# Optimization experiments

Hardware: AMD Instinct MI355X
Metric: run time of the kernel (lower is better)

The kernel has to match this reference:

```python
import jax, jax.numpy as jnp
import numpy as np

B, LQ, LA = 128, 128, 512
VOCAB, EMB, FILT, K = 50000, 300, 400, 3
EPS = 1e-8


def setup_inputs() -> dict:
    key = jax.random.key(0)
    kq, ka, ke, kw, kb, kW = jax.random.split(key, 6)
    questions = jax.random.randint(kq, (B, LQ), 0, VOCAB + 1, dtype=jnp.int32)
    answers = jax.random.randint(ka, (B, LA), 0, VOCAB + 1, dtype=jnp.int32)
    emb = jax.random.normal(ke, (VOCAB + 1, EMB), dtype=jnp.float32) * 0.1
    emb = emb.at[0].set(0.0)  # padding_idx=0
    fan_in = EMB * K
    bound = 1.0 / np.sqrt(fan_in)
    conv_w = jax.random.uniform(kw, (FILT, EMB, K), jnp.float32, -bound, bound)
    conv_b = jax.random.uniform(kb, (FILT,), jnp.float32, -bound, bound)
    W = jax.random.normal(kW, (FILT, FILT), dtype=jnp.float32)  # init.normal_(std=1)
    return {"questions": questions, "answers": answers, "emb": emb,
            "conv_w": conv_w, "conv_b": conv_b, "W": W}


def _encode(tokens, emb, conv_w, conv_b):
    # tokens [B,L] -> embed [B,L,E] -> transpose to NCH [B,E,L] -> conv1d pad=1
    x = emb[tokens].transpose(0, 2, 1)
    y = jax.lax.conv_general_dilated(
        x, conv_w, window_strides=(1,), padding=[(1, 1)],
        dimension_numbers=("NCH", "OIH", "NCH"))
    return y + conv_b[None, :, None]  # [B, FILT, L]


def reference(questions, answers, emb, conv_w, conv_b, W):
    Q = _encode(questions, emb, conv_w, conv_b)  # [B,F,Lq]
    A = _encode(answers, emb, conv_w, conv_b)    # [B,F,La]
    # G = tanh(Q^T W A)  -> [B, Lq, La]
    G = jnp.tanh(jnp.einsum("bfq,fg,bga->bqa", Q, W, A))
    roQ = jax.nn.softmax(jnp.max(G, axis=2), axis=1)  # [B,Lq]
    roA = jax.nn.softmax(jnp.max(G, axis=1), axis=1)  # [B,La]
    rQ = jnp.einsum("bfq,bq->bf", Q, roQ)  # [B,F]
    rA = jnp.einsum("bfa,ba->bf", A, roA)  # [B,F]
    nQ = jnp.maximum(jnp.linalg.norm(rQ, axis=1), EPS)
    nA = jnp.maximum(jnp.linalg.norm(rA, axis=1), EPS)
    return jnp.sum(rQ * rA, axis=1) / (nQ * nA)  # [B]
```

## Files before the change

### kernel.cpp

```cpp
#include <hip/hip_runtime.h>
#include <hip/hip_bf16.h>

#define BB   128
#define LQ   128
#define LA   512
#define EMBD 300
#define FILT 400
#define KW   3

#define NT   25
#define KC   30
#define KCF  13
#define MT   32

typedef unsigned short u16;
typedef unsigned int   u32;
typedef __attribute__((ext_vector_type(4))) int    i32x4;
typedef __attribute__((ext_vector_type(4))) float  f32x4;
typedef __attribute__((ext_vector_type(8))) __bf16 bf16x8;

__device__ __forceinline__ float b2f(u16 h){ return __uint_as_float(((u32)h) << 16); }
__device__ __forceinline__ u16 f2b(float f){
  u32 u = __float_as_uint(f);
  u32 r = (u + 0x7FFFu + ((u >> 16) & 1u)) >> 16;
  return (u16)r;
}
__device__ __forceinline__ u32 encf(float f){
  u32 u = __float_as_uint(f);
  return (u & 0x80000000u) ? ~u : (u | 0x80000000u);
}
__device__ __forceinline__ float decf(u32 k){
  u32 u = (k & 0x80000000u) ? (k ^ 0x80000000u) : ~k;
  return __uint_as_float(u);
}
__device__ __forceinline__ bf16x8 bzero(){
  i32x4 z; z.x = 0; z.y = 0; z.z = 0; z.w = 0;
  return __builtin_bit_cast(bf16x8, z);
}

__global__ void k_prep(const float* __restrict__ cw, const float* __restrict__ W,
                       u32* __restrict__ wTf, u32* __restrict__ wF){
  int idx = blockIdx.x * 256 + threadIdx.x;
  const int N1 = KC * NT * 64;
  const int N2 = KCF * NT * 64;
  if (idx < N1){
    int kc  = idx / (NT * 64);
    int rem = idx - kc * (NT * 64);
    int nt  = rem >> 6;
    int lane = rem & 63;
    int n = nt * 16 + (lane & 15);
    int quad = lane >> 4;
    u32 pack[4];
    #pragma unroll
    for (int d = 0; d < 4; d++){
      u16 h[2];
      #pragma unroll
      for (int s = 0; s < 2; s++){
        int kp = kc * 32 + quad * 8 + 2 * d + s;
        int kk = kp / 320, e = kp - kk * 320;
        float v = (e < EMBD) ? cw[(size_t)n * (EMBD * KW) + e * KW + kk] : 0.f;
        h[s] = f2b(v);
      }
      pack[d] = (u32)h[0] | ((u32)h[1] << 16);
    }
    i32x4 o; o.x = pack[0]; o.y = pack[1]; o.z = pack[2]; o.w = pack[3];
    *((i32x4*)wTf + idx) = o;
  } else if (idx < N1 + N2){
    int id2 = idx - N1;
    int kc  = id2 / (NT * 64);
    int rem = id2 - kc * (NT * 64);
    int nt  = rem >> 6;
    int lane = rem & 63;
    int n = nt * 16 + (lane & 15);
    int quad = lane >> 4;
    u32 pack[4];
    #pragma unroll
    for (int d = 0; d < 4; d++){
      u16 h[2];
      #pragma unroll
      for (int s = 0; s < 2; s++){
        int k = kc * 32 + quad * 8 + 2 * d + s;
        float v = (k < FILT) ? W[(size_t)k * FILT + n] : 0.f;
        h[s] = f2b(v);
      }
      pack[d] = (u32)h[0] | ((u32)h[1] << 16);
    }
    i32x4 o; o.x = pack[0]; o.y = pack[1]; o.z = pack[2]; o.w = pack[3];
    *((i32x4*)wF + id2) = o;
  }
}

__global__ __launch_bounds__(256) void k_encode_mfma(const int* __restrict__ toks,
    const float* __restrict__ emb, const u32* __restrict__ wTf,
    const float* __restrict__ bias, u16* __restrict__ out, int L){
  __shared__ u16 At[34 * 328];

  const int tid  = threadIdx.x;
  const int w    = tid >> 6;
  const int lane = tid & 63;
  const int col  = lane & 15;
  const int quad = lane >> 4;
  const int half = blockIdx.y;
  const int base_nt = half ? 13 : 0;
  const bool has4 = (half == 0) && (w == 0);
  const int row0 = blockIdx.x * MT;
  const int b    = row0 / L;
  const int l0   = row0 - b * L;

  int tk[10], cc[10], rws[10];
  #pragma unroll
  for (int u = 0; u < 10; u++){
    int idx = tid + 256 * u;
    tk[u] = -1; cc[u] = 0; rws[u] = 0;
    if (idx < 34 * 75){
      int r = idx / 75, c4 = idx - r * 75;
      int pos = l0 - 1 + r;
      cc[u] = c4;
      rws[u] = (r * 328 + c4 * 4) >> 1;
      if ((unsigned)pos < (unsigned)L) tk[u] = toks[b * L + pos];
    }
  }
  for (int i = tid; i < 34 * 328 / 2; i += 256) ((u32*)At)[i] = 0u;
  __syncthreads();
  {
    const float4* emb4 = (const float4*)emb;
    float4 v[10];
    #pragma unroll
    for (int u = 0; u < 10; u++)
      if (tk[u] >= 0) v[u] = emb4[(size_t)tk[u] * 75 + cc[u]];
    #pragma unroll
    for (int u = 0; u < 10; u++){
      if (tk[u] >= 0){
        u32 p0 = (u32)f2b(v[u].x) | ((u32)f2b(v[u].y) << 16);
        u32 p1 = (u32)f2b(v[u].z) | ((u32)f2b(v[u].w) << 16);
        ((u32*)At)[rws[u]]     = p0;
        ((u32*)At)[rws[u] + 1] = p1;
      }
    }
  }

  f32x4 acc[4][2];
  #pragma unroll
  for (int j = 0; j < 4; j++)
    #pragma unroll
    for (int mf = 0; mf < 2; mf++)
      acc[j][mf] = (f32x4){0.f, 0.f, 0.f, 0.f};

  __syncthreads();

  const i32x4* bbase = (const i32x4*)wTf + (size_t)(base_nt + w) * 64 + lane;
  i32x4 Bb[2][4];
  i32x4 Ab[2][2];
  {
    #pragma unroll
    for (int j = 0; j < 3; j++) Bb[0][j] = bbase[(4 * j) * 64];
    if (has4) Bb[0][3] = bbase[12 * 64];
    const int ebase0 = quad * 8;
    Ab[0][0] = *(const i32x4*)(At + (col) * 328 + ebase0);
    Ab[0][1] = *(const i32x4*)(At + (16 + col) * 328 + ebase0);
  }
  #pragma unroll
  for (int kc = 0; kc < KC; kc++){
    const int cur = kc & 1;
    if (kc + 1 < KC){
      const i32x4* s = bbase + (size_t)(kc + 1) * (NT * 64);
      #pragma unroll
      for (int j = 0; j < 3; j++) Bb[cur ^ 1][j] = s[(4 * j) * 64];
      if (has4) Bb[cur ^ 1][3] = s[12 * 64];
      const int kk1 = (kc + 1) / 10, e01 = ((kc + 1) - kk1 * 10) * 32;
      const int ebase1 = e01 + quad * 8;
      Ab[cur ^ 1][0] = *(const i32x4*)(At + (col + kk1) * 328 + ebase1);
      Ab[cur ^ 1][1] = *(const i32x4*)(At + (16 + col + kk1) * 328 + ebase1);
    }
    bf16x8 a0 = __builtin_bit_cast(bf16x8, Ab[cur][0]);
    bf16x8 a1 = __builtin_bit_cast(bf16x8, Ab[cur][1]);
    #pragma unroll
    for (int j = 0; j < 3; j++){
      bf16x8 bf = __builtin_bit_cast(bf16x8, Bb[cur][j]);
      acc[j][0] = __builtin_amdgcn_mfma_f32_16x16x32_bf16(a0, bf, acc[j][0], 0, 0, 0);
      acc[j][1] = __builtin_amdgcn_mfma_f32_16x16x32_bf16(a1, bf, acc[j][1], 0, 0, 0);
    }
    if (has4){
      bf16x8 bf = __builtin_bit_cast(bf16x8, Bb[cur][3]);
      acc[3][0] = __builtin_amdgcn_mfma_f32_16x16x32_bf16(a0, bf, acc[3][0], 0, 0, 0);
      acc[3][1] = __builtin_amdgcn_mfma_f32_16x16x32_bf16(a1, bf, acc[3][1], 0, 0, 0);
    }
  }

  #pragma unroll
  for (int j = 0; j < 4; j++){
    if (j == 3 && !has4) continue;
    int n = (base_nt + w + 4 * j) * 16 + col;
    float bv = bias[n];
    #pragma unroll
    for (int mf = 0; mf < 2; mf++){
      int rbase = row0 + mf * 16 + quad * 4;
      #pragma unroll
      for (int r = 0; r < 4; r++)
        out[(size_t)(rbase + r) * FILT + n] = f2b(acc[j][mf][r] + bv);
    }
  }
}

__global__ __launch_bounds__(256) void k_gemmT3(const u16* __restrict__ QT,
    const u32* __restrict__ wF, u16* __restrict__ T){
  const int tid  = threadIdx.x;
  const int w    = tid >> 6;
  const int lane = tid & 63;
  const int col  = lane & 15;
  const int quad = lane >> 4;
  const int half = blockIdx.y;
  const int base_nt = half ? 13 : 0;
  const bool has4 = (half == 0) && (w == 0);
  const int row0 = blockIdx.x * MT;

  f32x4 acc[4][2];
  #pragma unroll
  for (int j = 0; j < 4; j++)
    #pragma unroll
    for (int mf = 0; mf < 2; mf++)
      acc[j][mf] = (f32x4){0.f, 0.f, 0.f, 0.f};

  const u16* arow0 = QT + (size_t)(row0 + col) * FILT;
  const u16* arow1 = QT + (size_t)(row0 + 16 + col) * FILT;
  const i32x4* bbase = (const i32x4*)wF + (size_t)(base_nt + w) * 64 + lane;

  i32x4 Ab[2][2];
  i32x4 Bb[2][4];
  {
    int off = quad * 8;
    Ab[0][0] = *(const i32x4*)(arow0 + off);
    Ab[0][1] = *(const i32x4*)(arow1 + off);
    #pragma unroll
    for (int j = 0; j < 3; j++) Bb[0][j] = bbase[(4 * j) * 64];
    if (has4) Bb[0][3] = bbase[12 * 64];
  }
  #pragma unroll
  for (int kc = 0; kc < KCF; kc++){
    const int cur = kc & 1;
    if (kc + 1 < KCF){
      int off = (kc + 1) * 32 + quad * 8;
      Ab[cur ^ 1][0] = *(const i32x4*)(arow0 + off);
      Ab[cur ^ 1][1] = *(const i32x4*)(arow1 + off);
      const i32x4* s = bbase + (size_t)(kc + 1) * (NT * 64);
      #pragma unroll
      for (int j = 0; j < 3; j++) Bb[cur ^ 1][j] = s[(4 * j) * 64];
      if (has4) Bb[cur ^ 1][3] = s[12 * 64];
    }
    bf16x8 a0 = __builtin_bit_cast(bf16x8, Ab[cur][0]);
    bf16x8 a1 = __builtin_bit_cast(bf16x8, Ab[cur][1]);
    #pragma unroll
    for (int j = 0; j < 3; j++){
      bf16x8 bf = __builtin_bit_cast(bf16x8, Bb[cur][j]);
      acc[j][0] = __builtin_amdgcn_mfma_f32_16x16x32_bf16(a0, bf, acc[j][0], 0, 0, 0);
      acc[j][1] = __builtin_amdgcn_mfma_f32_16x16x32_bf16(a1, bf, acc[j][1], 0, 0, 0);
    }
    if (has4){
      bf16x8 bf = __builtin_bit_cast(bf16x8, Bb[cur][3]);
      acc[3][0] = __builtin_amdgcn_mfma_f32_16x16x32_bf16(a0, bf, acc[3][0], 0, 0, 0);
      acc[3][1] = __builtin_amdgcn_mfma_f32_16x16x32_bf16(a1, bf, acc[3][1], 0, 0, 0);
    }
  }

  #pragma unroll
  for (int j = 0; j < 4; j++){
    if (j == 3 && !has4) continue;
    int n = (base_nt + w + 4 * j) * 16 + col;
    #pragma unroll
    for (int mf = 0; mf < 2; mf++){
      int rbase = row0 + mf * 16 + quad * 4;
      #pragma unroll
      for (int r = 0; r < 4; r++)
        T[(size_t)(rbase + r) * FILT + n] = f2b(acc[j][mf][r]);
    }
  }
}

__global__ __launch_bounds__(256) void k_scores3(const u16* __restrict__ T,
    const u16* __restrict__ AT, u32* __restrict__ rowmaxE, u32* __restrict__ colmaxE){
  __shared__ float rpart[64][17];
  __shared__ float cpart[128][17];
  const int tid  = threadIdx.x;
  const int w    = tid >> 6;
  const int lane = tid & 63;
  const int col  = lane & 15;
  const int quad = lane >> 4;
  const int b    = blockIdx.y;
  const int a0   = blockIdx.x * 128;
  const int qt   = blockIdx.z * 4 + w;

  f32x4 acc[8];
  #pragma unroll
  for (int j = 0; j < 8; j++) acc[j] = (f32x4){0.f, 0.f, 0.f, 0.f};

  const u16* tr = T  + (size_t)(b * LQ + qt * 16 + col) * FILT;
  const u16* ar = AT + (size_t)(b * LA + a0 + col) * FILT;

  i32x4 Abuf[2], Bbuf[2][8];
  {
    int off = quad * 8;
    Abuf[0] = *(const i32x4*)(tr + off);
    #pragma unroll
    for (int j = 0; j < 8; j++)
      Bbuf[0][j] = *(const i32x4*)(ar + (size_t)(j * 16) * FILT + off);
  }
  #pragma unroll
  for (int kc = 0; kc < KCF; kc++){
    const int cur = kc & 1;
    if (kc + 1 < KCF){
      int off = (kc + 1) * 32 + quad * 8;
      Abuf[cur ^ 1] = *(const i32x4*)(tr + off);
      #pragma unroll
      for (int j = 0; j < 8; j++)
        Bbuf[cur ^ 1][j] = *(const i32x4*)(ar + (size_t)(j * 16) * FILT + off);
    }
    const bool live = (kc < 12) || (quad < 2);
    bf16x8 a0 = live ? __builtin_bit_cast(bf16x8, Abuf[cur]) : bzero();
    #pragma unroll
    for (int j = 0; j < 8; j++){
      bf16x8 bf = __builtin_bit_cast(bf16x8, Bbuf[cur][j]);
      acc[j] = __builtin_amdgcn_mfma_f32_16x16x32_bf16(a0, bf, acc[j], 0, 0, 0);
    }
  }

  #pragma unroll
  for (int r = 0; r < 4; r++){
    float m = acc[0][r];
    #pragma unroll
    for (int j = 1; j < 8; j++) m = fmaxf(m, acc[j][r]);
    rpart[w * 16 + quad * 4 + r][col] = m;
  }
  #pragma unroll
  for (int j = 0; j < 8; j++){
    float m = acc[j][0];
    #pragma unroll
    for (int r = 1; r < 4; r++) m = fmaxf(m, acc[j][r]);
    cpart[j * 16 + col][w * 4 + quad] = m;
  }
  __syncthreads();
  if (tid < 64){
    float m = rpart[tid][0];
    #pragma unroll
    for (int g = 1; g < 16; g++) m = fmaxf(m, rpart[tid][g]);
    atomicMax(&rowmaxE[b * LQ + blockIdx.z * 64 + tid], encf(m));
  } else if (tid < 192){
    int a = tid - 64;
    float m2 = cpart[a][0];
    #pragma unroll
    for (int g = 1; g < 16; g++) m2 = fmaxf(m2, cpart[a][g]);
    atomicMax(&colmaxE[b * LA + a0 + a], encf(m2));
  }
  if (tid >= 192 && tid < 256){
    int a = tid - 128;
    float m2 = cpart[a][0];
    #pragma unroll
    for (int g = 1; g < 16; g++) m2 = fmaxf(m2, cpart[a][g]);
    atomicMax(&colmaxE[b * LA + a0 + a], encf(m2));
  }
}

__global__ __launch_bounds__(256) void k_soft(const u32* __restrict__ rme,
    const u32* __restrict__ cme, float* __restrict__ roq, float* __restrict__ roa){
  __shared__ float sq[128];
  __shared__ float sa[512];
  __shared__ float red[4];
  int b = blockIdx.x, tid = threadIdx.x;
  if (tid < 128) sq[tid] = tanhf(decf(rme[b * LQ + tid]));
  sa[tid]       = tanhf(decf(cme[b * LA + tid]));
  sa[tid + 256] = tanhf(decf(cme[b * LA + 256 + tid]));
  __syncthreads();
  if (tid < 64){
    float m = fmaxf(sq[tid], sq[tid + 64]);
    #pragma unroll
    for (int off = 32; off; off >>= 1) m = fmaxf(m, __shfl_down(m, off));
    if (tid == 0) red[0] = m;
  } else if (tid < 128){
    int l = tid - 64;
    float m = sa[l];
    #pragma unroll
    for (int i = 1; i < 8; i++) m = fmaxf(m, sa[l + 64 * i]);
    #pragma unroll
    for (int off = 32; off; off >>= 1) m = fmaxf(m, __shfl_down(m, off));
    if (l == 0) red[1] = m;
  }
  __syncthreads();
  float mq = red[0], ma = red[1];
  if (tid < 128) sq[tid] = __expf(sq[tid] - mq);
  sa[tid]       = __expf(sa[tid] - ma);
  sa[tid + 256] = __expf(sa[tid + 256] - ma);
  __syncthreads();
  if (tid < 64){
    float s = sq[tid] + sq[tid + 64];
    #pragma unroll
    for (int off = 32; off; off >>= 1) s += __shfl_down(s, off);
    if (tid == 0) red[2] = s;
  } else if (tid < 128){
    int l = tid - 64;
    float s = 0.f;
    #pragma unroll
    for (int i = 0; i < 8; i++) s += sa[l + 64 * i];
    #pragma unroll
    for (int off = 32; off; off >>= 1) s += __shfl_down(s, off);
    if (l == 0) red[3] = s;
  }
  __syncthreads();
  float iq = 1.f / red[2], ia = 1.f / red[3];
  if (tid < 128) roq[b * LQ + tid] = sq[tid] * iq;
  roa[b * LA + tid]       = sa[tid] * ia;
  roa[b * LA + 256 + tid] = sa[tid + 256] * ia;
}

__global__ __launch_bounds__(256) void k_pool(const u16* __restrict__ QT,
    const u16* __restrict__ AT, const float* __restrict__ roq, const float* __restrict__ roa,
    float* __restrict__ rqp, float* __restrict__ rap){
  __shared__ float wq[32];
  __shared__ float wa[128];
  int s = blockIdx.x, b = blockIdx.y, tid = threadIdx.x;
  if (tid < 32) wq[tid] = roq[b * LQ + s * 32 + tid];
  if (tid >= 128 && tid < 256) wa[tid - 128] = roa[b * LA + s * 128 + (tid - 128)];
  __syncthreads();
  if (tid < FILT / 2){
    const u32* qp = (const u32*)(QT + (size_t)(b * LQ + s * 32) * FILT) + tid;
    const u32* ap = (const u32*)(AT + (size_t)(b * LA + s * 128) * FILT) + tid;
    float rq0 = 0.f, rq1 = 0.f, ra0 = 0.f, ra1 = 0.f;
    for (int q = 0; q < 32; q++){
      u32 u = qp[q * (FILT / 2)];
      float wv = wq[q];
      rq0 += __uint_as_float(u << 16) * wv;
      rq1 += __uint_as_float(u & 0xFFFF0000u) * wv;
    }
    for (int a = 0; a < 128; a++){
      u32 u = ap[a * (FILT / 2)];
      float wv = wa[a];
      ra0 += __uint_as_float(u << 16) * wv;
      ra1 += __uint_as_float(u & 0xFFFF0000u) * wv;
    }
    size_t base = ((size_t)b * 4 + s) * FILT + 2 * tid;
    rqp[base] = rq0; rqp[base + 1] = rq1;
    rap[base] = ra0; rap[base + 1] = ra1;
  }
}

__global__ __launch_bounds__(256) void k_cos(const float* __restrict__ rqp,
    const float* __restrict__ rap, float* __restrict__ outp){
  __shared__ float rd[4], r1[4], r2[4];
  int b = blockIdx.x, tid = threadIdx.x;
  int lane = tid & 63, w = tid >> 6;
  float d = 0.f, n1 = 0.f, n2 = 0.f;
  for (int f = tid; f < FILT; f += 256){
    size_t base = (size_t)b * 4 * FILT + f;
    float rq = rqp[base] + rqp[base + FILT] + rqp[base + 2 * FILT] + rqp[base + 3 * FILT];
    float ra = rap[base] + rap[base + FILT] + rap[base + 2 * FILT] + rap[base + 3 * FILT];
    d += rq * ra; n1 += rq * rq; n2 += ra * ra;
  }
  #pragma unroll
  for (int off = 32; off; off >>= 1){
    d  += __shfl_down(d, off);
    n1 += __shfl_down(n1, off);
    n2 += __shfl_down(n2, off);
  }
  if (lane == 0){ rd[w] = d; r1[w] = n1; r2[w] = n2; }
  __syncthreads();
  if (tid == 0){
    float D  = rd[0] + rd[1] + rd[2] + rd[3];
    float N1 = r1[0] + r1[1] + r1[2] + r1[3];
    float N2 = r2[0] + r2[1] + r2[2] + r2[3];
    outp[b] = D / (fmaxf(sqrtf(N1), 1e-8f) * fmaxf(sqrtf(N2), 1e-8f));
  }
}

extern "C" void kernel_launch(void* const* d_in, const int* in_sizes, int n_in,
                              void* d_out, int out_size, void* d_ws, size_t ws_size,
                              hipStream_t stream){
  const int*   qtok = (const int*)d_in[0];
  const int*   atok = (const int*)d_in[1];
  const float* emb  = (const float*)d_in[2];
  const float* cw   = (const float*)d_in[3];
  const float* cb   = (const float*)d_in[4];
  const float* W    = (const float*)d_in[5];
  float* outp = (float*)d_out;

  char* ws = (char*)d_ws;
  size_t off = 0;
  auto alloc = [&](size_t bytes) -> char* {
    char* p = ws + off;
    off = (off + bytes + 255) & ~(size_t)255;
    return p;
  };
  u32*   wTf = (u32*)alloc((size_t)KC * NT * 64 * 16);
  u32*   wF  = (u32*)alloc((size_t)KCF * NT * 64 * 16);
  u16*   QT  = (u16*)alloc((size_t)BB * LQ * FILT * 2);
  u16*   AT  = (u16*)alloc((size_t)BB * LA * FILT * 2);
  u16*   T   = (u16*)alloc((size_t)BB * LQ * FILT * 2);
  u32*   rme = (u32*)alloc((size_t)BB * LQ * 4);
  u32*   cme = (u32*)alloc((size_t)BB * LA * 4);
  float* roq = (float*)alloc((size_t)BB * LQ * 4);
  float* roa = (float*)alloc((size_t)BB * LA * 4);
  float* rqp = (float*)alloc((size_t)BB * 4 * FILT * 4);
  float* rap = (float*)alloc((size_t)BB * 4 * FILT * 4);

  hipMemsetAsync(rme, 0, (size_t)BB * LQ * 4 + (size_t)BB * LA * 4, stream);

  const int NPREP = KC * NT * 64 + KCF * NT * 64;
  k_prep<<<dim3((NPREP + 255) / 256), 256, 0, stream>>>(cw, W, wTf, wF);
  k_encode_mfma<<<dim3(BB * LQ / MT, 2), 256, 0, stream>>>(qtok, emb, wTf, cb, QT, LQ);
  k_encode_mfma<<<dim3(BB * LA / MT, 2), 256, 0, stream>>>(atok, emb, wTf, cb, AT, LA);
  k_gemmT3<<<dim3(BB * LQ / MT, 2), 256, 0, stream>>>(QT, wF, T);
  k_scores3<<<dim3(LA / 128, BB, 2), 256, 0, stream>>>(T, AT, rme, cme);
  k_soft<<<dim3(BB), 256, 0, stream>>>(rme, cme, roq, roa);
  k_pool<<<dim3(4, BB), 256, 0, stream>>>(QT, AT, roq, roa, rqp, rap);
  k_cos<<<dim3(BB), 256, 0, stream>>>(rqp, rap, outp);
}
```

Measured before the change: 265.4 us.

## Fuse W-projection into score kernel and merge softmax, pooling, cosine tail

Replaces the separate Q·W GEMM and score kernels with one kernel. It computes the projected Q tile into shared memory and immediately multiplies it against A rows to produce row and column maxima. This removes the global T buffer round trip. The softmax, weighted pooling and cosine kernels are merged into a single per-batch kernel, removing intermediate global buffers and launches. The cost is that each (z, qh) block recomputes its Q·W tile twice across z, and the grid is now 512 blocks, which may limit parallelism.

```diff
diff --git a/kernel.cpp b/kernel.cpp
--- a/kernel.cpp
+++ b/kernel.cpp
@@ -19,7 +19,6 @@
 typedef __attribute__((ext_vector_type(4))) float  f32x4;
 typedef __attribute__((ext_vector_type(8))) __bf16 bf16x8;
 
-__device__ __forceinline__ float b2f(u16 h){ return __uint_as_float(((u32)h) << 16); }
 __device__ __forceinline__ u16 f2b(float f){
   u32 u = __float_as_uint(f);
   u32 r = (u + 0x7FFFu + ((u >> 16) & 1u)) >> 16;
@@ -202,256 +201,206 @@
   }
 }
 
-__global__ __launch_bounds__(256) void k_gemmT3(const u16* __restrict__ QT,
-    const u32* __restrict__ wF, u16* __restrict__ T){
+__global__ __launch_bounds__(512) void k_mid(const u16* __restrict__ QT,
+    const u32* __restrict__ wF, const u16* __restrict__ AT,
+    u32* __restrict__ rme, u32* __restrict__ cme){
+  __shared__ u16 Ts[64 * 408];
+  __shared__ float cpart[256][5];
   const int tid  = threadIdx.x;
   const int w    = tid >> 6;
   const int lane = tid & 63;
   const int col  = lane & 15;
   const int quad = lane >> 4;
-  const int half = blockIdx.y;
-  const int base_nt = half ? 13 : 0;
-  const bool has4 = (half == 0) && (w == 0);
-  const int row0 = blockIdx.x * MT;
-
-  f32x4 acc[4][2];
-  #pragma unroll
-  for (int j = 0; j < 4; j++)
-    #pragma unroll
-    for (int mf = 0; mf < 2; mf++)
-      acc[j][mf] = (f32x4){0.f, 0.f, 0.f, 0.f};
-
-  const u16* arow0 = QT + (size_t)(row0 + col) * FILT;
-  const u16* arow1 = QT + (size_t)(row0 + 16 + col) * FILT;
-  const i32x4* bbase = (const i32x4*)wF + (size_t)(base_nt + w) * 64 + lane;
-
-  i32x4 Ab[2][2];
-  i32x4 Bb[2][4];
+  const int z    = blockIdx.x;
+  const int qh   = blockIdx.y;
+  const int b    = blockIdx.z;
+  const int wq   = w & 3;
+  const int wh   = w >> 2;
+
   {
-    int off = quad * 8;
-    Ab[0][0] = *(const i32x4*)(arow0 + off);
-    Ab[0][1] = *(const i32x4*)(arow1 + off);
-    #pragma unroll
-    for (int j = 0; j < 3; j++) Bb[0][j] = bbase[(4 * j) * 64];
-    if (has4) Bb[0][3] = bbase[12 * 64];
-  }
-  #pragma unroll
-  for (int kc = 0; kc < KCF; kc++){
-    const int cur = kc & 1;
-    if (kc + 1 < KCF){
-      int off = (kc + 1) * 32 + quad * 8;
-      Ab[cur ^ 1][0] = *(const i32x4*)(arow0 + off);
-      Ab[cur ^ 1][1] = *(const i32x4*)(arow1 + off);
-      const i32x4* s = bbase + (size_t)(kc + 1) * (NT * 64);
-      #pragma unroll
-      for (int j = 0; j < 3; j++) Bb[cur ^ 1][j] = s[(4 * j) * 64];
-      if (has4) Bb[cur ^ 1][3] = s[12 * 64];
-    }
-    bf16x8 a0 = __builtin_bit_cast(bf16x8, Ab[cur][0]);
-    bf16x8 a1 = __builtin_bit_cast(bf16x8, Ab[cur][1]);
-    #pragma unroll
-    for (int j = 0; j < 3; j++){
-      bf16x8 bf = __builtin_bit_cast(bf16x8, Bb[cur][j]);
-      acc[j][0] = __builtin_amdgcn_mfma_f32_16x16x32_bf16(a0, bf, acc[j][0], 0, 0, 0);
-      acc[j][1] = __builtin_amdgcn_mfma_f32_16x16x32_bf16(a1, bf, acc[j][1], 0, 0, 0);
-    }
-    if (has4){
-      bf16x8 bf = __builtin_bit_cast(bf16x8, Bb[cur][3]);
-      acc[3][0] = __builtin_amdgcn_mfma_f32_16x16x32_bf16(a0, bf, acc[3][0], 0, 0, 0);
-      acc[3][1] = __builtin_amdgcn_mfma_f32_16x16x32_bf16(a1, bf, acc[3][1], 0, 0, 0);
-    }
-  }
-
-  #pragma unroll
-  for (int j = 0; j < 4; j++){
-    if (j == 3 && !has4) continue;
-    int n = (base_nt + w + 4 * j) * 16 + col;
-    #pragma unroll
-    for (int mf = 0; mf < 2; mf++){
-      int rbase = row0 + mf * 16 + quad * 4;
-      #pragma unroll
-      for (int r = 0; r < 4; r++)
-        T[(size_t)(rbase + r) * FILT + n] = f2b(acc[j][mf][r]);
-    }
-  }
-}
-
-__global__ __launch_bounds__(256) void k_scores3(const u16* __restrict__ T,
-    const u16* __restrict__ AT, u32* __restrict__ rowmaxE, u32* __restrict__ colmaxE){
-  __shared__ float rpart[64][17];
-  __shared__ float cpart[128][17];
-  const int tid  = threadIdx.x;
-  const int w    = tid >> 6;
-  const int lane = tid & 63;
-  const int col  = lane & 15;
-  const int quad = lane >> 4;
-  const int b    = blockIdx.y;
-  const int a0   = blockIdx.x * 128;
-  const int qt   = blockIdx.z * 4 + w;
-
-  f32x4 acc[8];
-  #pragma unroll
-  for (int j = 0; j < 8; j++) acc[j] = (f32x4){0.f, 0.f, 0.f, 0.f};
-
-  const u16* tr = T  + (size_t)(b * LQ + qt * 16 + col) * FILT;
-  const u16* ar = AT + (size_t)(b * LA + a0 + col) * FILT;
-
-  i32x4 Abuf[2], Bbuf[2][8];
+    const int bnt = wh ? 13 : 0;
+    const int cnt = wh ? 12 : 13;
+    const u16* arow = QT + (size_t)(b * LQ + qh * 64 + wq * 16 + col) * FILT;
+    const i32x4* wFp = (const i32x4*)wF;
+    for (int ntc = 0; ntc < 3; ntc++){
+      const int nleft = cnt - ntc * 5;
+      f32x4 acc[5];
+      #pragma unroll
+      for (int j = 0; j < 5; j++) acc[j] = (f32x4){0.f, 0.f, 0.f, 0.f};
+      i32x4 Ab[2], Bb[2][5];
+      Ab[0] = *(const i32x4*)(arow + quad * 8);
+      #pragma unroll
+      for (int j = 0; j < 5; j++)
+        if (j < nleft) Bb[0][j] = wFp[(size_t)(bnt + ntc * 5 + j) * 64 + lane];
+      for (int kc = 0; kc < KCF; kc++){
+        const int cur = kc & 1;
+        if (kc + 1 < KCF){
+          Ab[cur ^ 1] = *(const i32x4*)(arow + (kc + 1) * 32 + quad * 8);
+          #pragma unroll
+          for (int j = 0; j < 5; j++)
+            if (j < nleft)
+              Bb[cur ^ 1][j] = wFp[((size_t)(kc + 1) * NT + bnt + ntc * 5 + j) * 64 + lane];
+        }
+        bf16x8 a = __builtin_bit_cast(bf16x8, Ab[cur]);
+        #pragma unroll
+        for (int j = 0; j < 5; j++)
+          if (j < nleft)
+            acc[j] = __builtin_amdgcn_mfma_f32_16x16x32_bf16(a,
+                       __builtin_bit_cast(bf16x8, Bb[cur][j]), acc[j], 0, 0, 0);
+      }
+      #pragma unroll
+      for (int j = 0; j < 5; j++){
+        if (j < nleft){
+          int g = (bnt + ntc * 5 + j) * 16 + col;
+          #pragma unroll
+          for (int r = 0; r < 4; r++)
+            Ts[(wq * 16 + quad * 4 + r) * 408 + g] = f2b(acc[j][r]);
+        }
+      }
+    }
+  }
+  __syncthreads();
+
+  float rm[4];
+  #pragma unroll
+  for (int r = 0; r < 4; r++) rm[r] = -3.4e38f;
+  const u16* Tsrow = Ts + (wq * 16 + col) * 408;
+  for (int atg = 0; atg < 2; atg++){
+    f32x4 acc[4];
+    #pragma unroll
+    for (int i = 0; i < 4; i++) acc[i] = (f32x4){0.f, 0.f, 0.f, 0.f};
+    const u16* ar[4];
+    #pragma unroll
+    for (int i = 0; i < 4; i++)
+      ar[i] = AT + (size_t)(b * LA + z * 256 + (wh * 8 + atg * 4 + i) * 16 + col) * FILT;
+    i32x4 Ab2[2], Bb2[2][4];
+    Ab2[0] = *(const i32x4*)(Tsrow + quad * 8);
+    #pragma unroll
+    for (int i = 0; i < 4; i++) Bb2[0][i] = *(const i32x4*)(ar[i] + quad * 8);
+    for (int kc = 0; kc < KCF; kc++){
+      const int cur = kc & 1;
+      if (kc + 1 < KCF){
+        int off = (kc + 1) * 32 + quad * 8;
+        Ab2[cur ^ 1] = *(const i32x4*)(Tsrow + off);
+        #pragma unroll
+        for (int i = 0; i < 4; i++) Bb2[cur ^ 1][i] = *(const i32x4*)(ar[i] + off);
+      }
+      const bool live = (kc < 12) || (quad < 2);
+      bf16x8 a = live ? __builtin_bit_cast(bf16x8, Ab2[cur]) : bzero();
+      #pragma unroll
+      for (int i = 0; i < 4; i++)
+        acc[i] = __builtin_amdgcn_mfma_f32_16x16x32_bf16(a,
+                   __builtin_bit_cast(bf16x8, Bb2[cur][i]), acc[i], 0, 0, 0);
+    }
+    #pragma unroll
+    for (int i = 0; i < 4; i++){
+      float cmx = fmaxf(fmaxf(acc[i][0], acc[i][1]), fmaxf(acc[i][2], acc[i][3]));
+      cmx = fmaxf(cmx, __shfl_xor(cmx, 16));
+      cmx = fmaxf(cmx, __shfl_xor(cmx, 32));
+      if (quad == 0) cpart[(wh * 8 + atg * 4 + i) * 16 + col][wq] = cmx;
+      #pragma unroll
+      for (int r = 0; r < 4; r++) rm[r] = fmaxf(rm[r], acc[i][r]);
+    }
+  }
+  #pragma unroll
+  for (int r = 0; r < 4; r++){
+    float m = rm[r];
+    m = fmaxf(m, __shfl_xor(m, 1));
+    m = fmaxf(m, __shfl_xor(m, 2));
+    m = fmaxf(m, __shfl_xor(m, 4));
+    m = fmaxf(m, __shfl_xor(m, 8));
+    if (col == 0)
+      atomicMax(&rme[b * LQ + qh * 64 + wq * 16 + quad * 4 + r], encf(m));
+  }
+  __syncthreads();
+  if (tid < 256){
+    float m = cpart[tid][0];
+    #pragma unroll
+    for (int s = 1; s < 4; s++) m = fmaxf(m, cpart[tid][s]);
+    atomicMax(&cme[b * LA + z * 256 + tid], encf(m));
+  }
+}
+
+__global__ __launch_bounds__(512) void k_tail(const u16* __restrict__ QT,
+    const u16* __restrict__ AT, const u32* __restrict__ rme,
+    const u32* __restrict__ cme, float* __restrict__ outp){
+  __shared__ float roq[128];
+  __shared__ float roa[512];
+  __shared__ float red[4];
+  __shared__ float rqp[8][400];
+  __shared__ float rap[8][400];
+  __shared__ float fin[8][3];
+  const int tid = threadIdx.x, w = tid >> 6, lane = tid & 63;
+  const int b = blockIdx.x;
+  if (tid < 128) roq[tid] = tanhf(decf(rme[b * LQ + tid]));
+  roa[tid] = tanhf(decf(cme[b * LA + tid]));
+  __syncthreads();
+  if (w == 0){
+    float m = fmaxf(roq[lane], roq[lane + 64]);
+    #pragma unroll
+    for (int off = 32; off; off >>= 1) m = fmaxf(m, __shfl_down(m, off));
+    if (lane == 0) red[0] = m;
+  } else if (w == 1){
+    float m = roa[lane];
+    #pragma unroll
+    for (int i = 1; i < 8; i++) m = fmaxf(m, roa[lane + 64 * i]);
+    #pragma unroll
+    for (int off = 32; off; off >>= 1) m = fmaxf(m, __shfl_down(m, off));
+    if (lane == 0) red[1] = m;
+  }
+  __syncthreads();
+  if (tid < 128) roq[tid] = __expf(roq[tid] - red[0]);
+  roa[tid] = __expf(roa[tid] - red[1]);
+  __syncthreads();
+  if (w == 0){
+    float s = roq[lane] + roq[lane + 64];
+    #pragma unroll
+    for (int off = 32; off; off >>= 1) s += __shfl_down(s, off);
+    if (lane == 0) red[2] = s;
+  } else if (w == 1){
+    float s = 0.f;
+    #pragma unroll
+    for (int i = 0; i < 8; i++) s += roa[lane + 64 * i];
+    #pragma unroll
+    for (int off = 32; off; off >>= 1) s += __shfl_down(s, off);
+    if (lane == 0) red[3] = s;
+  }
+  __syncthreads();
+  if (tid < 128) roq[tid] *= (1.f / red[2]);
+  roa[tid] *= (1.f / red[3]);
+  __syncthreads();
   {
-    int off = quad * 8;
-    Abuf[0] = *(const i32x4*)(tr + off);
-    #pragma unroll
-    for (int j = 0; j < 8; j++)
-      Bbuf[0][j] = *(const i32x4*)(ar + (size_t)(j * 16) * FILT + off);
-  }
-  #pragma unroll
-  for (int kc = 0; kc < KCF; kc++){
-    const int cur = kc & 1;
-    if (kc + 1 < KCF){
-      int off = (kc + 1) * 32 + quad * 8;
-      Abuf[cur ^ 1] = *(const i32x4*)(tr + off);
-      #pragma unroll
-      for (int j = 0; j < 8; j++)
-        Bbuf[cur ^ 1][j] = *(const i32x4*)(ar + (size_t)(j * 16) * FILT + off);
-    }
-    const bool live = (kc < 12) || (quad < 2);
-    bf16x8 a0 = live ? __builtin_bit_cast(bf16x8, Abuf[cur]) : bzero();
-    #pragma unroll
-    for (int j = 0; j < 8; j++){
-      bf16x8 bf = __builtin_bit_cast(bf16x8, Bbuf[cur][j]);
-      acc[j] = __builtin_amdgcn_mfma_f32_16x16x32_bf16(a0, bf, acc[j], 0, 0, 0);
-    }
-  }
-
-  #pragma unroll
-  for (int r = 0; r < 4; r++){
-    float m = acc[0][r];
-    #pragma unroll
-    for (int j = 1; j < 8; j++) m = fmaxf(m, acc[j][r]);
-    rpart[w * 16 + quad * 4 + r][col] = m;
-  }
-  #pragma unroll
-  for (int j = 0; j < 8; j++){
-    float m = acc[j][0];
-    #pragma unroll
-    for (int r = 1; r < 4; r++) m = fmaxf(m, acc[j][r]);
-    cpart[j * 16 + col][w * 4 + quad] = m;
-  }
-  __syncthreads();
-  if (tid < 64){
-    float m = rpart[tid][0];
-    #pragma unroll
-    for (int g = 1; g < 16; g++) m = fmaxf(m, rpart[tid][g]);
-    atomicMax(&rowmaxE[b * LQ + blockIdx.z * 64 + tid], encf(m));
-  } else if (tid < 192){
-    int a = tid - 64;
-    float m2 = cpart[a][0];
-    #pragma unroll
-    for (int g = 1; g < 16; g++) m2 = fmaxf(m2, cpart[a][g]);
-    atomicMax(&colmaxE[b * LA + a0 + a], encf(m2));
-  }
-  if (tid >= 192 && tid < 256){
-    int a = tid - 128;
-    float m2 = cpart[a][0];
-    #pragma unroll
-    for (int g = 1; g < 16; g++) m2 = fmaxf(m2, cpart[a][g]);
-    atomicMax(&colmaxE[b * LA + a0 + a], encf(m2));
-  }
-}
-
-__global__ __launch_bounds__(256) void k_soft(const u32* __restrict__ rme,
-    const u32* __restrict__ cme, float* __restrict__ roq, float* __restrict__ roa){
-  __shared__ float sq[128];
-  __shared__ float sa[512];
-  __shared__ float red[4];
-  int b = blockIdx.x, tid = threadIdx.x;
-  if (tid < 128) sq[tid] = tanhf(decf(rme[b * LQ + tid]));
-  sa[tid]       = tanhf(decf(cme[b * LA + tid]));
-  sa[tid + 256] = tanhf(decf(cme[b * LA + 256 + tid]));
-  __syncthreads();
-  if (tid < 64){
-    float m = fmaxf(sq[tid], sq[tid + 64]);
-    #pragma unroll
-    for (int off = 32; off; off >>= 1) m = fmaxf(m, __shfl_down(m, off));
-    if (tid == 0) red[0] = m;
-  } else if (tid < 128){
-    int l = tid - 64;
-    float m = sa[l];
-    #pragma unroll
-    for (int i = 1; i < 8; i++) m = fmaxf(m, sa[l + 64 * i]);
-    #pragma unroll
-    for (int off = 32; off; off >>= 1) m = fmaxf(m, __shfl_down(m, off));
-    if (l == 0) red[1] = m;
-  }
-  __syncthreads();
-  float mq = red[0], ma = red[1];
-  if (tid < 128) sq[tid] = __expf(sq[tid] - mq);
-  sa[tid]       = __expf(sa[tid] - ma);
-  sa[tid + 256] = __expf(sa[tid + 256] - ma);
-  __syncthreads();
-  if (tid < 64){
-    float s = sq[tid] + sq[tid + 64];
-    #pragma unroll
-    for (int off = 32; off; off >>= 1) s += __shfl_down(s, off);
-    if (tid == 0) red[2] = s;
-  } else if (tid < 128){
-    int l = tid - 64;
-    float s = 0.f;
-    #pragma unroll
-    for (int i = 0; i < 8; i++) s += sa[l + 64 * i];
-    #pragma unroll
-    for (int off = 32; off; off >>= 1) s += __shfl_down(s, off);
-    if (l == 0) red[3] = s;
-  }
-  __syncthreads();
-  float iq = 1.f / red[2], ia = 1.f / red[3];
-  if (tid < 128) roq[b * LQ + tid] = sq[tid] * iq;
-  roa[b * LA + tid]       = sa[tid] * ia;
-  roa[b * LA + 256 + tid] = sa[tid + 256] * ia;
-}
-
-__global__ __launch_bounds__(256) void k_pool(const u16* __restrict__ QT,
-    const u16* __restrict__ AT, const float* __restrict__ roq, const float* __restrict__ roa,
-    float* __restrict__ rqp, float* __restrict__ rap){
-  __shared__ float wq[32];
-  __shared__ float wa[128];
-  int s = blockIdx.x, b = blockIdx.y, tid = threadIdx.x;
-  if (tid < 32) wq[tid] = roq[b * LQ + s * 32 + tid];
-  if (tid >= 128 && tid < 256) wa[tid - 128] = roa[b * LA + s * 128 + (tid - 128)];
-  __syncthreads();
-  if (tid < FILT / 2){
-    const u32* qp = (const u32*)(QT + (size_t)(b * LQ + s * 32) * FILT) + tid;
-    const u32* ap = (const u32*)(AT + (size_t)(b * LA + s * 128) * FILT) + tid;
-    float rq0 = 0.f, rq1 = 0.f, ra0 = 0.f, ra1 = 0.f;
-    for (int q = 0; q < 32; q++){
-      u32 u = qp[q * (FILT / 2)];
-      float wv = wq[q];
-      rq0 += __uint_as_float(u << 16) * wv;
-      rq1 += __uint_as_float(u & 0xFFFF0000u) * wv;
-    }
-    for (int a = 0; a < 128; a++){
-      u32 u = ap[a * (FILT / 2)];
-      float wv = wa[a];
-      ra0 += __uint_as_float(u << 16) * wv;
-      ra1 += __uint_as_float(u & 0xFFFF0000u) * wv;
-    }
-    size_t base = ((size_t)b * 4 + s) * FILT + 2 * tid;
-    rqp[base] = rq0; rqp[base + 1] = rq1;
-    rap[base] = ra0; rap[base + 1] = ra1;
-  }
-}
-
-__global__ __launch_bounds__(256) void k_cos(const float* __restrict__ rqp,
-    const float* __restrict__ rap, float* __restrict__ outp){
-  __shared__ float rd[4], r1[4], r2[4];
-  int b = blockIdx.x, tid = threadIdx.x;
-  int lane = tid & 63, w = tid >> 6;
+    const u32* qp = (const u32*)(QT + (size_t)(b * LQ + w * 16) * FILT);
+    const u32* ap = (const u32*)(AT + (size_t)(b * LA + w * 64) * FILT);
+    #pragma unroll
+    for (int i = 0; i < 4; i++){
+      int g = lane + 64 * i;
+      if (g < FILT / 2){
+        float rq0 = 0.f, rq1 = 0.f, ra0 = 0.f, ra1 = 0.f;
+        for (int q = 0; q < 16; q++){
+          u32 u = qp[q * (FILT / 2) + g];
+          float wv = roq[w * 16 + q];
+          rq0 += __uint_as_float(u << 16) * wv;
+          rq1 += __uint_as_float(u & 0xFFFF0000u) * wv;
+        }
+        for (int a = 0; a < 64; a++){
+          u32 u = ap[a * (FILT / 2) + g];
+          float wv = roa[w * 64 + a];
+          ra0 += __uint_as_float(u << 16) * wv;
+          ra1 += __uint_as_float(u & 0xFFFF0000u) * wv;
+        }
+        rqp[w][2 * g] = rq0; rqp[w][2 * g + 1] = rq1;
+        rap[w][2 * g] = ra0; rap[w][2 * g + 1] = ra1;
+      }
+    }
+  }
+  __syncthreads();
   float d = 0.f, n1 = 0.f, n2 = 0.f;
-  for (int f = tid; f < FILT; f += 256){
-    size_t base = (size_t)b * 4 * FILT + f;
-    float rq = rqp[base] + rqp[base + FILT] + rqp[base + 2 * FILT] + rqp[base + 3 * FILT];
-    float ra = rap[base] + rap[base + FILT] + rap[base + 2 * FILT] + rap[base + 3 * FILT];
-    d += rq * ra; n1 += rq * rq; n2 += ra * ra;
+  if (tid < FILT){
+    float rq = 0.f, ra = 0.f;
+    #pragma unroll
+    for (int s = 0; s < 8; s++){ rq += rqp[s][tid]; ra += rap[s][tid]; }
+    d = rq * ra; n1 = rq * rq; n2 = ra * ra;
   }
   #pragma unroll
   for (int off = 32; off; off >>= 1){
@@ -459,12 +408,12 @@
     n1 += __shfl_down(n1, off);
     n2 += __shfl_down(n2, off);
   }
-  if (lane == 0){ rd[w] = d; r1[w] = n1; r2[w] = n2; }
+  if (lane == 0){ fin[w][0] = d; fin[w][1] = n1; fin[w][2] = n2; }
   __syncthreads();
   if (tid == 0){
-    float D  = rd[0] + rd[1] + rd[2] + rd[3];
-    float N1 = r1[0] + r1[1] + r1[2] + r1[3];
-    float N2 = r2[0] + r2[1] + r2[2] + r2[3];
+    float D = 0.f, N1 = 0.f, N2 = 0.f;
+    #pragma unroll
+    for (int s = 0; s < 8; s++){ D += fin[s][0]; N1 += fin[s][1]; N2 += fin[s][2]; }
     outp[b] = D / (fmaxf(sqrtf(N1), 1e-8f) * fmaxf(sqrtf(N2), 1e-8f));
   }
 }
@@ -491,13 +440,8 @@
   u32*   wF  = (u32*)alloc((size_t)KCF * NT * 64 * 16);
   u16*   QT  = (u16*)alloc((size_t)BB * LQ * FILT * 2);
   u16*   AT  = (u16*)alloc((size_t)BB * LA * FILT * 2);
-  u16*   T   = (u16*)alloc((size_t)BB * LQ * FILT * 2);
   u32*   rme = (u32*)alloc((size_t)BB * LQ * 4);
   u32*   cme = (u32*)alloc((size_t)BB * LA * 4);
-  float* roq = (float*)alloc((size_t)BB * LQ * 4);
-  float* roa = (float*)alloc((size_t)BB * LA * 4);
-  float* rqp = (float*)alloc((size_t)BB * 4 * FILT * 4);
-  float* rap = (float*)alloc((size_t)BB * 4 * FILT * 4);
 
   hipMemsetAsync(rme, 0, (size_t)BB * LQ * 4 + (size_t)BB * LA * 4, stream);
 
@@ -505,9 +449,6 @@
   k_prep<<<dim3((NPREP + 255) / 256), 256, 0, stream>>>(cw, W, wTf, wF);
   k_encode_mfma<<<dim3(BB * LQ / MT, 2), 256, 0, stream>>>(qtok, emb, wTf, cb, QT, LQ);
   k_encode_mfma<<<dim3(BB * LA / MT, 2), 256, 0, stream>>>(atok, emb, wTf, cb, AT, LA);
-  k_gemmT3<<<dim3(BB * LQ / MT, 2), 256, 0, stream>>>(QT, wF, T);
-  k_scores3<<<dim3(LA / 128, BB, 2), 256, 0, stream>>>(T, AT, rme, cme);
-  k_soft<<<dim3(BB), 256, 0, stream>>>(rme, cme, roq, roa);
-  k_pool<<<dim3(4, BB), 256, 0, stream>>>(QT, AT, roq, roa, rqp, rap);
-  k_cos<<<dim3(BB), 256, 0, stream>>>(rqp, rap, outp);
-}
+  k_mid<<<dim3(2, 2, BB), 512, 0, stream>>>(QT, wF, AT, rme, cme);
+  k_tail<<<dim3(BB), 512, 0, stream>>>(QT, AT, rme, cme, outp);
+}
```

After: 276.2 us. 4.1% more time.
